# Optimization experiments

Hardware: AMD Instinct MI355X
Metric: run time of the kernel (lower is better)

The kernel has to match this reference:

```python
import math
import jax, jax.numpy as jnp
import numpy as np

D, H, NB, L, K = 45, 256, 6, 2, 8          # features, hidden, maf blocks, made hidden layers, spline bins
M = 3 * K - 1                               # params per feature (tails='linear')
TAIL = -math.log(1e-6)                      # tail_bound = -log(alpha)
MIN_BW = MIN_BH = MIN_D = 1e-3


def _masks():
    # nflows MADE sequential degrees (random_mask=False)
    d_in = np.arange(1, D + 1)
    d_h = (np.arange(H) % (D - 1)) + 1
    m0 = (d_h[:, None] >= d_in[None, :]).astype(np.float32)   # [H, D]
    mh = (d_h[:, None] >= d_h[None, :]).astype(np.float32)    # [H, H]
    d_out = np.repeat(d_in, M)                                 # nflows tile(): each degree repeated M times
    mf = (d_out[:, None] > d_h[None, :]).astype(np.float32)   # [D*M, H], strict for output layer
    return jnp.asarray(m0), jnp.asarray(mh), jnp.asarray(mf)


def _rq_spline(x, params):
    # x: [B, D]; params: [B, D, M]. unconstrained_rational_quadratic_spline, tails='linear'.
    uw = params[..., :K] / math.sqrt(H)        # nflows divides by sqrt(hidden_features)
    uh = params[..., K:2 * K] / math.sqrt(H)
    const = math.log(math.exp(1.0 - MIN_D) - 1.0)
    ud = jnp.pad(params[..., 2 * K:], ((0, 0), (0, 0), (1, 1)), constant_values=const)  # [B,D,K+1]
    inside = (x >= -TAIL) & (x <= TAIL)
    xc = jnp.clip(x, -TAIL, TAIL)

    def bin_edges(u, mn):
        p = jax.nn.softmax(u, -1)
        p = mn + (1.0 - mn * K) * p
        c = jnp.pad(jnp.cumsum(p, -1), ((0, 0), (0, 0), (1, 0)))
        c = 2.0 * TAIL * c - TAIL
        c = c.at[..., 0].set(-TAIL).at[..., -1].set(TAIL)
        return c, c[..., 1:] - c[..., :-1]

    cw, w = bin_edges(uw, MIN_BW)              # cumwidths [B,D,K+1], widths [B,D,K]
    ch, h = bin_edges(uh, MIN_BH)
    d = MIN_D + jax.nn.softplus(ud)            # derivatives [B,D,K+1]

    idx = jnp.clip(jnp.sum((xc[..., None] >= cw), -1) - 1, 0, K - 1)[..., None]
    g = lambda a: jnp.take_along_axis(a, idx, -1)[..., 0]
    icw, ibw, ich, ih = g(cw[..., :-1]), g(w), g(ch[..., :-1]), g(h)
    idelta = g(h / w)
    id0, id1 = g(d[..., :-1]), g(d[..., 1:])

    th = (xc - icw) / ibw
    th1 = th * (1.0 - th)
    den = idelta + (id0 + id1 - 2.0 * idelta) * th1
    y = ich + ih * (idelta * th * th + id0 * th1) / den
    lad = jnp.log(idelta * idelta * (id1 * th * th + 2.0 * idelta * th1 + id0 * (1.0 - th) ** 2)) - 2.0 * jnp.log(den)
    return jnp.where(inside, y, x), jnp.where(inside, lad, 0.0)


def setup_inputs() -> dict:
    key = jax.random.key(0)
    ks = jax.random.split(key, 10)
    B, s = 32768, 0.02
    return {
        "x": jax.random.normal(ks[0], (B, D), jnp.float32),
        "cond": jax.random.normal(ks[1], (B, 1), jnp.float32),
        "W0": jax.random.normal(ks[2], (NB, H, D), jnp.float32) * s,
        "b0": jax.random.normal(ks[3], (NB, H), jnp.float32) * s,
        "Wc": jax.random.normal(ks[4], (NB, H, 1), jnp.float32) * s,
        "bc": jax.random.normal(ks[5], (NB, H), jnp.float32) * s,
        "Wh": jax.random.normal(ks[6], (NB, L, H, H), jnp.float32) * s,
        "bh": jax.random.normal(ks[7], (NB, L, H), jnp.float32) * s,
        "Wf": jax.random.normal(ks[8], (NB, D * M, H), jnp.float32) * s,
        "bf": jax.random.normal(ks[9], (NB, D * M), jnp.float32) * s,
    }


def reference(x, cond, W0, b0, Wc, bc, Wh, bh, Wf, bf):
    m0, mh, mf = _masks()
    z = x
    ld = jnp.zeros(x.shape[0], x.dtype)
    for b in range(NB):  # CompositeTransform of NB MAF blocks
        hid = z @ (W0[b] * m0).T + b0[b] + cond @ Wc[b].T + bc[b]
        for l in range(L):  # MaskedFeedforwardBlock: linear -> ReLU (dropout=0, no BN)
            hid = jax.nn.relu(hid @ (Wh[b, l] * mh).T + bh[b, l])
        params = (hid @ (Wf[b] * mf).T + bf[b]).reshape(z.shape[0], D, M)
        z, lad = _rq_spline(z, params)
        ld = ld + lad.sum(-1)
    log_z = 0.5 * D * math.log(2.0 * math.pi)
    return -0.5 * jnp.sum(z * z, axis=1) - log_z + ld
```

## Files before the change

### kernel.cpp

```cpp
#include <hip/hip_runtime.h>


typedef __bf16 bf16;
typedef __bf16 bf16x8 __attribute__((ext_vector_type(8)));
typedef float  f32x16 __attribute__((ext_vector_type(16)));

#define TAILF  13.815510557964274f
#define LOGZ   41.352233994210265f

#define WS_W0M   0
#define WS_WHM   196608
#define WS_WFM   1769472
#define WS_BEFF  5210112
#define WS_BFP   5216256
#define WS_WCC   5243136
#define WS_NEED  5249280

#define N_W0  (6*256*64)
#define N_WH  (6*2*256*256)
#define N_WF  (6*5*224*256)
#define N_PREP (N_W0 + N_WH + N_WF)

__global__ void prep_all(const float* __restrict__ W0, const float* __restrict__ b0,
                         const float* __restrict__ Wc, const float* __restrict__ bc,
                         const float* __restrict__ Wh, const float* __restrict__ Wf,
                         const float* __restrict__ bfv,
                         bf16* __restrict__ W0m, bf16* __restrict__ Whm,
                         bf16* __restrict__ Wfm,
                         float* __restrict__ beff, float* __restrict__ bfp,
                         float* __restrict__ Wcc)
{
    int idx = blockIdx.x * 256 + threadIdx.x;
    if (idx < N_W0) {
        int j = idx & 7, lane = (idx >> 3) & 63, chunk = idx >> 9;
        int kt = chunk & 3, cg = (chunk >> 2) & 7, b = chunk >> 5;
        int col = cg * 32 + (lane & 31);
        int k   = kt * 16 + (lane >> 5) * 8 + j;
        float v = 0.f;
        if (k < 45 && (col % 44) >= k)
            v = W0[(b * 256 + col) * 45 + k];
        W0m[idx] = (bf16)v;
        if (k == 0) {
            beff[b * 256 + col] = b0[b * 256 + col] + bc[b * 256 + col];
            Wcc[b * 256 + col]  = Wc[b * 256 + col];
        }
    } else if (idx < N_W0 + N_WH) {
        int id = idx - N_W0;
        int j = id & 7, lane = (id >> 3) & 63, chunk = id >> 9;
        int kt = chunk & 15, cg = (chunk >> 4) & 7, bl = chunk >> 7;
        int col = cg * 32 + (lane & 31);
        int k   = kt * 16 + (lane >> 5) * 8 + j;
        float v = ((col % 44) >= (k % 44)) ? Wh[bl * 65536 + col * 256 + k] : 0.f;
        Whm[id] = (bf16)v;
    } else if (idx < N_PREP) {
        int id = idx - (N_W0 + N_WH);
        int j = id & 7, lane = (id >> 3) & 63, chunk = id >> 9;
        int kt = chunk & 15, t2 = chunk >> 4;
        int cg = t2 % 7, bg = t2 / 7;
        int b  = bg / 5, g = bg - 5 * b;
        int col = cg * 32 + (lane & 31);
        int k   = kt * 16 + (lane >> 5) * 8 + j;
        int f   = 9 * g + col / 23;
        int m   = col - (col / 23) * 23;
        bool valid = (col < 207);
        float v = 0.f;
        if (valid && (f > (k % 44)))
            v = Wf[(b * 1035 + f * 23 + m) * 256 + k];
        Wfm[id] = (bf16)v;
        if (k == 0)
            bfp[bg * 224 + col] = valid ? bfv[b * 1035 + f * 23 + m] : 0.f;
    }
}

#define SO_ZF    0
#define SO_ZB    11776
#define SO_HIDA  20992
#define SO_PBUF  54784
#define SO_COND  81408
#define SO_LD    81664
#define SMEM_BYTES 81920

template<int KT, int NACT, int MODE, int LIMIT>
__device__ __forceinline__ void gemm32(
    const bf16* Asrc, int lda,
    const bf16* __restrict__ Wp,
    const float* __restrict__ bias, const float* __restrict__ wcol,
    const float* condl, bf16* dst, int ldd,
    int w, int lane, bool preEpiSync)
{
    const bool act  = (w < NACT);
    const int  l31  = lane & 31;
    const int  kh8  = (lane >> 5) * 8;
    const bf16* Bp  = Wp + ((size_t)w * KT) * 512 + lane * 8;
    const bf16* Ap  = Asrc + l31 * lda + kh8;

    f32x16 acc0 = {}, acc1 = {};
    constexpr int CH = (KT < 8) ? KT : 8;
    #pragma unroll
    for (int khb = 0; khb < KT / CH; ++khb) {
        bf16x8 bq[CH];
        if (act) {
            #pragma unroll
            for (int c = 0; c < CH; ++c)
                bq[c] = *reinterpret_cast<const bf16x8*>(Bp + (khb * CH + c) * 512);
            #pragma unroll
            for (int c = 0; c < CH; ++c) {
                int kt = khb * CH + c;
                bf16x8 a0 = *reinterpret_cast<const bf16x8*>(Ap + kt * 16);
                bf16x8 a1 = *reinterpret_cast<const bf16x8*>(Ap + 32 * lda + kt * 16);
                acc0 = __builtin_amdgcn_mfma_f32_32x32x16_bf16(a0, bq[c], acc0, 0, 0, 0);
                acc1 = __builtin_amdgcn_mfma_f32_32x32x16_bf16(a1, bq[c], acc1, 0, 0, 0);
            }
        }
    }

    if (preEpiSync) __syncthreads();

    if (act) {
        const int col = w * 32 + l31;
        if (NACT == 8 || col < LIMIT) {
            const float bv  = bias[col];
            const float wcv = (MODE == 0) ? wcol[col] : 0.f;
            #pragma unroll
            for (int r = 0; r < 16; ++r) {
                int row = (r & 3) + 8 * (r >> 2) + (kh8 >> 1);
                float v0 = acc0[r] + bv;
                float v1 = acc1[r] + bv;
                if (MODE == 0) { v0 += condl[row] * wcv; v1 += condl[row + 32] * wcv; }
                if (MODE == 1) { v0 = fmaxf(v0, 0.f);   v1 = fmaxf(v1, 0.f); }
                dst[row * ldd + col]        = (bf16)v0;
                dst[(row + 32) * ldd + col] = (bf16)v1;
            }
        }
    }
    __syncthreads();
}

template<int NF>
__device__ __forceinline__ void do_spline(int fb, float* zf, bf16* zb,
                                          const bf16* pbuf, float* ldl, int t)
{
    for (int task = t; task < 64 * NF; task += 512) {
        int r  = task / NF;
        int fl = task - r * NF;
        const bf16* pp = pbuf + r * 208 + fl * 23;
        float P[23];
        #pragma unroll
        for (int m = 0; m < 23; ++m) P[m] = (float)pp[m];

        float xin = zf[r * 46 + fb + fl];
        float xc  = fminf(fmaxf(xin, -TAILF), TAILF);
        bool inside = (xin >= -TAILF) && (xin <= TAILF);

        float mw = P[0];
        #pragma unroll
        for (int i = 1; i < 8; ++i) mw = fmaxf(mw, P[i]);
        float ew[8], sw = 0.f;
        #pragma unroll
        for (int i = 0; i < 8; ++i) { ew[i] = __expf((P[i] - mw) * 0.0625f); sw += ew[i]; }
        float rws = 0.992f / sw;
        float cw[9]; cw[0] = -TAILF;
        #pragma unroll
        for (int i = 0; i < 8; ++i)
            cw[i + 1] = cw[i] + 2.f * TAILF * (1e-3f + ew[i] * rws);
        cw[8] = TAILF;
        float wb[8];
        #pragma unroll
        for (int i = 0; i < 8; ++i) wb[i] = cw[i + 1] - cw[i];

        float mh = P[8];
        #pragma unroll
        for (int i = 1; i < 8; ++i) mh = fmaxf(mh, P[8 + i]);
        float eh[8], sh = 0.f;
        #pragma unroll
        for (int i = 0; i < 8; ++i) { eh[i] = __expf((P[8 + i] - mh) * 0.0625f); sh += eh[i]; }
        float rhs = 0.992f / sh;
        float ch[9]; ch[0] = -TAILF;
        #pragma unroll
        for (int i = 0; i < 8; ++i)
            ch[i + 1] = ch[i] + 2.f * TAILF * (1e-3f + eh[i] * rhs);
        ch[8] = TAILF;
        float hb[8];
        #pragma unroll
        for (int i = 0; i < 8; ++i) hb[i] = ch[i + 1] - ch[i];

        float dd[9];
        dd[0] = 1.0f; dd[8] = 1.0f;
        #pragma unroll
        for (int i = 1; i < 8; ++i)
            dd[i] = 1e-3f + __logf(1.f + __expf(P[15 + i]));

        float icw = cw[0], ich = ch[0], ibw = wb[0], ibh = hb[0];
        float id0 = dd[0], id1 = dd[1];
        #pragma unroll
        for (int i = 1; i < 8; ++i) {
            bool ge = xc >= cw[i];
            icw = ge ? cw[i] : icw;  ich = ge ? ch[i] : ich;
            ibw = ge ? wb[i] : ibw;  ibh = ge ? hb[i] : ibh;
            id0 = ge ? dd[i] : id0;  id1 = ge ? dd[i + 1] : id1;
        }

        float th  = (xc - icw) / ibw;
        float th1 = th * (1.f - th);
        float dl  = ibh / ibw;
        float den = dl + (id0 + id1 - 2.f * dl) * th1;
        float yy  = ich + ibh * (dl * th * th + id0 * th1) / den;
        float num = dl * dl * (id1 * th * th + 2.f * dl * th1
                               + id0 * (1.f - th) * (1.f - th));
        float lad = __logf(num) - 2.f * __logf(den);

        if (inside) {
            zf[r * 46 + fb + fl] = yy;
            zb[r * 72 + fb + fl] = (bf16)yy;
            atomicAdd(&ldl[r], lad);
        }
    }
}

__global__ __launch_bounds__(512, 4) void maf_main(
    const float* __restrict__ x, const float* __restrict__ cond,
    const float* __restrict__ bh_all,
    const bf16* __restrict__ W0m, const bf16* __restrict__ Whm,
    const bf16* __restrict__ Wfm,
    const float* __restrict__ beff, const float* __restrict__ bfp,
    const float* __restrict__ Wcc,
    float* __restrict__ out, int B)
{
    extern __shared__ char smem[];
    float* zf    = (float*)(smem + SO_ZF);
    bf16*  zb    = (bf16*)(smem + SO_ZB);
    bf16*  hidA  = (bf16*)(smem + SO_HIDA);
    bf16*  pbuf  = (bf16*)(smem + SO_PBUF);
    float* condl = (float*)(smem + SO_COND);
    float* ldl   = (float*)(smem + SO_LD);

    const int t    = threadIdx.x;
    const int r0   = blockIdx.x * 64;
    const int w    = t >> 6;
    const int lane = t & 63;

    for (int i = t; i < 64 * 27; i += 512) {
        int r = i / 27, c = i - (i / 27) * 27;
        zb[r * 72 + 45 + c] = (bf16)0.f;
    }
    for (int i = t; i < 64 * 45; i += 512) {
        int r = i / 45, f = i - (i / 45) * 45;
        float v = (r0 + r < B) ? x[(size_t)(r0 + r) * 45 + f] : 0.f;
        zf[r * 46 + f] = v;
        zb[r * 72 + f] = (bf16)v;
    }
    if (t < 64) {
        condl[t] = (r0 + t < B) ? cond[r0 + t] : 0.f;
        ldl[t]   = 0.f;
    }
    __syncthreads();

    #pragma unroll 1
    for (int b = 0; b < 6; ++b) {
        gemm32<4, 8, 0, 256>(zb, 72, W0m + b * 16384,
                             beff + b * 256, Wcc + b * 256, condl,
                             hidA, 264, w, lane, false);
        #pragma unroll 1
        for (int l = 0; l < 2; ++l)
            gemm32<16, 8, 1, 256>(hidA, 264, Whm + (b * 2 + l) * 65536,
                                  bh_all + (b * 2 + l) * 256, nullptr, condl,
                                  hidA, 264, w, lane, true);
        #pragma unroll 1
        for (int g = 0; g < 5; ++g) {
            gemm32<16, 7, 2, 208>(hidA, 264, Wfm + (size_t)(b * 5 + g) * 57344,
                                  bfp + (b * 5 + g) * 224, nullptr, condl,
                                  pbuf, 208, w, lane, false);
            do_spline<9>(g * 9, zf, zb, pbuf, ldl, t);
            __syncthreads();
        }
    }

    if (t < 64 && r0 + t < B) {
        float s = 0.f;
        #pragma unroll
        for (int f = 0; f < 45; ++f) { float v = zf[t * 46 + f]; s += v * v; }
        out[r0 + t] = -0.5f * s - LOGZ + ldl[t];
    }
}

extern "C" void kernel_launch(void* const* d_in, const int* in_sizes, int n_in,
                              void* d_out, int out_size, void* d_ws, size_t ws_size,
                              hipStream_t stream)
{
    const float* x    = (const float*)d_in[0];
    const float* cond = (const float*)d_in[1];
    const float* W0   = (const float*)d_in[2];
    const float* b0   = (const float*)d_in[3];
    const float* Wc   = (const float*)d_in[4];
    const float* bc   = (const float*)d_in[5];
    const float* Wh   = (const float*)d_in[6];
    const float* bh   = (const float*)d_in[7];
    const float* Wf   = (const float*)d_in[8];
    const float* bfv  = (const float*)d_in[9];
    float* out = (float*)d_out;

    const int B = in_sizes[0] / 45;
    if (ws_size < (size_t)WS_NEED) return;

    char* ws = (char*)d_ws;
    bf16*  W0m  = (bf16*)(ws + WS_W0M);
    bf16*  Whm  = (bf16*)(ws + WS_WHM);
    bf16*  Wfm  = (bf16*)(ws + WS_WFM);
    float* beff = (float*)(ws + WS_BEFF);
    float* bfp  = (float*)(ws + WS_BFP);
    float* Wcc  = (float*)(ws + WS_WCC);

    prep_all<<<(N_PREP + 255) / 256, 256, 0, stream>>>(
        W0, b0, Wc, bc, Wh, Wf, bfv, W0m, Whm, Wfm, beff, bfp, Wcc);

    (void)hipFuncSetAttribute((const void*)maf_main,
                              hipFuncAttributeMaxDynamicSharedMemorySize,
                              SMEM_BYTES);

    const int nwg = (B + 63) / 64;
    maf_main<<<nwg, 512, SMEM_BYTES, stream>>>(
        x, cond, bh, W0m, Whm, Wfm, beff, bfp, Wcc, out, B);
}
```

Before: 375.0 us.

## Transpose MFMA operand roles, vectorize epilogue, pad spline params, drop softmax max

Weights become the MFMA A operand and activations the B operand. Each wave now owns 32 rows and two 32-column tiles, so the epilogue writes packed bf16x4 rows with vectorized bias loads. The first layer reads the fp32 z buffer directly, which removes the separate bf16 copy of z, and cuts its K tiles from 4 to 3. Spline params are padded to 24 per feature so they can be read with 16-byte loads. The spline also drops the softmax max-subtraction and swaps divisions for reciprocals; this risks overflow if the logits are large and adds some rounding error.

Result: slower. 435.5 us (+16.1%).

```diff
diff --git a/kernel.cpp b/kernel.cpp
--- a/kernel.cpp
+++ b/kernel.cpp
@@ -2,23 +2,25 @@
 
 
 typedef __bf16 bf16;
+typedef __bf16 bf16x4 __attribute__((ext_vector_type(4)));
 typedef __bf16 bf16x8 __attribute__((ext_vector_type(8)));
+typedef float  f32x4  __attribute__((ext_vector_type(4)));
 typedef float  f32x16 __attribute__((ext_vector_type(16)));
 
 #define TAILF  13.815510557964274f
 #define LOGZ   41.352233994210265f
 
 #define WS_W0M   0
-#define WS_WHM   196608
-#define WS_WFM   1769472
-#define WS_BEFF  5210112
-#define WS_BFP   5216256
-#define WS_WCC   5243136
-#define WS_NEED  5249280
-
-#define N_W0  (6*256*64)
+#define WS_WHM   147456
+#define WS_WFM   1720320
+#define WS_BEFF  5160960
+#define WS_BFP   5167104
+#define WS_WCC   5193984
+#define WS_NEED  5200128
+
+#define N_W0  (6*8*3*512)
 #define N_WH  (6*2*256*256)
-#define N_WF  (6*5*224*256)
+#define N_WF  (30*7*16*512)
 #define N_PREP (N_W0 + N_WH + N_WF)
 
 __global__ void prep_all(const float* __restrict__ W0, const float* __restrict__ b0,
@@ -33,8 +35,8 @@
     int idx = blockIdx.x * 256 + threadIdx.x;
     if (idx < N_W0) {
         int j = idx & 7, lane = (idx >> 3) & 63, chunk = idx >> 9;
-        int kt = chunk & 3, cg = (chunk >> 2) & 7, b = chunk >> 5;
-        int col = cg * 32 + (lane & 31);
+        int kt = chunk % 3, t = (chunk / 3) & 7, b = chunk / 24;
+        int col = t * 32 + (lane & 31);
         int k   = kt * 16 + (lane >> 5) * 8 + j;
         float v = 0.f;
         if (k < 45 && (col % 44) >= k)
@@ -47,8 +49,8 @@
     } else if (idx < N_W0 + N_WH) {
         int id = idx - N_W0;
         int j = id & 7, lane = (id >> 3) & 63, chunk = id >> 9;
-        int kt = chunk & 15, cg = (chunk >> 4) & 7, bl = chunk >> 7;
-        int col = cg * 32 + (lane & 31);
+        int kt = chunk & 15, t = (chunk >> 4) & 7, bl = chunk >> 7;
+        int col = t * 32 + (lane & 31);
         int k   = kt * 16 + (lane >> 5) * 8 + j;
         float v = ((col % 44) >= (k % 44)) ? Wh[bl * 65536 + col * 256 + k] : 0.f;
         Whm[id] = (bf16)v;
@@ -56,13 +58,13 @@
         int id = idx - (N_W0 + N_WH);
         int j = id & 7, lane = (id >> 3) & 63, chunk = id >> 9;
         int kt = chunk & 15, t2 = chunk >> 4;
-        int cg = t2 % 7, bg = t2 / 7;
+        int t  = t2 % 7, bg = t2 / 7;
         int b  = bg / 5, g = bg - 5 * b;
-        int col = cg * 32 + (lane & 31);
+        int col = t * 32 + (lane & 31);
         int k   = kt * 16 + (lane >> 5) * 8 + j;
-        int f   = 9 * g + col / 23;
-        int m   = col - (col / 23) * 23;
-        bool valid = (col < 207);
+        int f   = 9 * g + col / 24;
+        int m   = col - (col / 24) * 24;
+        bool valid = (col < 216) && (m < 23);
         float v = 0.f;
         if (valid && (f > (k % 44)))
             v = Wf[(b * 1035 + f * 23 + m) * 256 + k];
@@ -73,92 +75,131 @@
 }
 
 #define SO_ZF    0
-#define SO_ZB    11776
-#define SO_HIDA  20992
-#define SO_PBUF  54784
-#define SO_COND  81408
-#define SO_LD    81664
-#define SMEM_BYTES 81920
-
-template<int KT, int NACT, int MODE, int LIMIT>
+#define SO_HIDA  12288
+#define SO_PBUF  46080
+#define SO_COND  73728
+#define SO_LD    73984
+#define SMEM_BYTES 74240
+
+template<int KT, int NT, int MODE, bool F32B, int LIMIT>
 __device__ __forceinline__ void gemm32(
-    const bf16* Asrc, int lda,
+    const void* Bact, int ldb,
     const bf16* __restrict__ Wp,
     const float* __restrict__ bias, const float* __restrict__ wcol,
-    const float* condl, bf16* dst, int ldd,
+    float condv, bf16* dst, int ldd,
     int w, int lane, bool preEpiSync)
 {
-    const bool act  = (w < NACT);
-    const int  l31  = lane & 31;
-    const int  kh8  = (lane >> 5) * 8;
-    const bf16* Bp  = Wp + ((size_t)w * KT) * 512 + lane * 8;
-    const bf16* Ap  = Asrc + l31 * lda + kh8;
+    const int cg  = w & 3;
+    const int rg  = w >> 2;
+    const int l31 = lane & 31;
+    const int q   = lane >> 5;
+    const int t0  = cg * 2, t1 = cg * 2 + 1;
+    const bool has1 = (NT == 8) || (t1 < NT);
+    const int row = rg * 32 + l31;
+
+    const bf16*  Bp  = (const bf16*)Bact + row * ldb + q * 8;
+    const float* Bpf = (const float*)Bact + row * ldb + q * 8;
+    const bf16*  A0  = Wp + ((size_t)t0 * KT) * 512 + lane * 8;
+    const bf16*  A1  = Wp + ((size_t)t1 * KT) * 512 + lane * 8;
 
     f32x16 acc0 = {}, acc1 = {};
-    constexpr int CH = (KT < 8) ? KT : 8;
+    constexpr int CH = (KT < 4) ? KT : 4;
     #pragma unroll
-    for (int khb = 0; khb < KT / CH; ++khb) {
-        bf16x8 bq[CH];
-        if (act) {
-            #pragma unroll
-            for (int c = 0; c < CH; ++c)
-                bq[c] = *reinterpret_cast<const bf16x8*>(Bp + (khb * CH + c) * 512);
-            #pragma unroll
-            for (int c = 0; c < CH; ++c) {
-                int kt = khb * CH + c;
-                bf16x8 a0 = *reinterpret_cast<const bf16x8*>(Ap + kt * 16);
-                bf16x8 a1 = *reinterpret_cast<const bf16x8*>(Ap + 32 * lda + kt * 16);
-                acc0 = __builtin_amdgcn_mfma_f32_32x32x16_bf16(a0, bq[c], acc0, 0, 0, 0);
-                acc1 = __builtin_amdgcn_mfma_f32_32x32x16_bf16(a1, bq[c], acc1, 0, 0, 0);
+    for (int kb = 0; kb < KT / CH; ++kb) {
+        bf16x8 wq0[CH], wq1[CH];
+        #pragma unroll
+        for (int c = 0; c < CH; ++c) {
+            wq0[c] = *reinterpret_cast<const bf16x8*>(A0 + (kb * CH + c) * 512);
+            if (has1)
+                wq1[c] = *reinterpret_cast<const bf16x8*>(A1 + (kb * CH + c) * 512);
+        }
+        #pragma unroll
+        for (int c = 0; c < CH; ++c) {
+            const int kt = kb * CH + c;
+            bf16x8 bfrag;
+            if constexpr (F32B) {
+                f32x4 fa = *reinterpret_cast<const f32x4*>(Bpf + kt * 16);
+                f32x4 fb = *reinterpret_cast<const f32x4*>(Bpf + kt * 16 + 4);
+                bfrag = (bf16x8){(bf16)fa[0], (bf16)fa[1], (bf16)fa[2], (bf16)fa[3],
+                                 (bf16)fb[0], (bf16)fb[1], (bf16)fb[2], (bf16)fb[3]};
+            } else {
+                bfrag = *reinterpret_cast<const bf16x8*>(Bp + kt * 16);
             }
+            acc0 = __builtin_amdgcn_mfma_f32_32x32x16_bf16(wq0[c], bfrag, acc0, 0, 0, 0);
+            if (has1)
+                acc1 = __builtin_amdgcn_mfma_f32_32x32x16_bf16(wq1[c], bfrag, acc1, 0, 0, 0);
         }
     }
 
     if (preEpiSync) __syncthreads();
 
-    if (act) {
-        const int col = w * 32 + l31;
-        if (NACT == 8 || col < LIMIT) {
-            const float bv  = bias[col];
-            const float wcv = (MODE == 0) ? wcol[col] : 0.f;
-            #pragma unroll
-            for (int r = 0; r < 16; ++r) {
-                int row = (r & 3) + 8 * (r >> 2) + (kh8 >> 1);
-                float v0 = acc0[r] + bv;
-                float v1 = acc1[r] + bv;
-                if (MODE == 0) { v0 += condl[row] * wcv; v1 += condl[row + 32] * wcv; }
-                if (MODE == 1) { v0 = fmaxf(v0, 0.f);   v1 = fmaxf(v1, 0.f); }
-                dst[row * ldd + col]        = (bf16)v0;
-                dst[(row + 32) * ldd + col] = (bf16)v1;
+    bf16* drow = dst + row * ldd;
+    #pragma unroll
+    for (int rr = 0; rr < 4; ++rr) {
+        {
+            const int colb = t0 * 32 + rr * 8 + q * 4;
+            if (LIMIT == 256 || colb < LIMIT) {
+                f32x4 bv = *reinterpret_cast<const f32x4*>(bias + colb);
+                f32x4 wc = {};
+                if (MODE == 0) wc = *reinterpret_cast<const f32x4*>(wcol + colb);
+                bf16x4 pk;
+                #pragma unroll
+                for (int i = 0; i < 4; ++i) {
+                    float v = acc0[rr * 4 + i] + bv[i];
+                    if (MODE == 0) v += condv * wc[i];
+                    if (MODE == 1) v = fmaxf(v, 0.f);
+                    pk[i] = (bf16)v;
+                }
+                *reinterpret_cast<bf16x4*>(drow + colb) = pk;
             }
         }
+        if (has1) {
+            const int colb = t1 * 32 + rr * 8 + q * 4;
+            if (LIMIT == 256 || colb < LIMIT) {
+                f32x4 bv = *reinterpret_cast<const f32x4*>(bias + colb);
+                f32x4 wc = {};
+                if (MODE == 0) wc = *reinterpret_cast<const f32x4*>(wcol + colb);
+                bf16x4 pk;
+                #pragma unroll
+                for (int i = 0; i < 4; ++i) {
+                    float v = acc1[rr * 4 + i] + bv[i];
+                    if (MODE == 0) v += condv * wc[i];
+                    if (MODE == 1) v = fmaxf(v, 0.f);
+                    pk[i] = (bf16)v;
+                }
+                *reinterpret_cast<bf16x4*>(drow + colb) = pk;
+            }
+        }
     }
     __syncthreads();
 }
 
-template<int NF>
-__device__ __forceinline__ void do_spline(int fb, float* zf, bf16* zb,
+__device__ __forceinline__ void do_spline(int fb, float* zf,
                                           const bf16* pbuf, float* ldl, int t)
 {
-    for (int task = t; task < 64 * NF; task += 512) {
-        int r  = task / NF;
-        int fl = task - r * NF;
-        const bf16* pp = pbuf + r * 208 + fl * 23;
-        float P[23];
-        #pragma unroll
-        for (int m = 0; m < 23; ++m) P[m] = (float)pp[m];
-
-        float xin = zf[r * 46 + fb + fl];
+    for (int task = t; task < 64 * 9; task += 512) {
+        int r  = task / 9;
+        int fl = task - r * 9;
+        const bf16* pp = pbuf + r * 216 + fl * 24;
+        bf16x8 p0 = *reinterpret_cast<const bf16x8*>(pp);
+        bf16x8 p1 = *reinterpret_cast<const bf16x8*>(pp + 8);
+        bf16x8 p2 = *reinterpret_cast<const bf16x8*>(pp + 16);
+        float P[24];
+        #pragma unroll
+        for (int m = 0; m < 8; ++m) {
+            P[m]      = (float)p0[m];
+            P[8 + m]  = (float)p1[m];
+            P[16 + m] = (float)p2[m];
+        }
+
+        float xin = zf[r * 48 + fb + fl];
         float xc  = fminf(fmaxf(xin, -TAILF), TAILF);
         bool inside = (xin >= -TAILF) && (xin <= TAILF);
 
-        float mw = P[0];
-        #pragma unroll
-        for (int i = 1; i < 8; ++i) mw = fmaxf(mw, P[i]);
         float ew[8], sw = 0.f;
         #pragma unroll
-        for (int i = 0; i < 8; ++i) { ew[i] = __expf((P[i] - mw) * 0.0625f); sw += ew[i]; }
-        float rws = 0.992f / sw;
+        for (int i = 0; i < 8; ++i) { ew[i] = __expf(P[i] * 0.0625f); sw += ew[i]; }
+        float rws = 0.992f * __frcp_rn(sw);
         float cw[9]; cw[0] = -TAILF;
         #pragma unroll
         for (int i = 0; i < 8; ++i)
@@ -168,13 +209,10 @@
         #pragma unroll
         for (int i = 0; i < 8; ++i) wb[i] = cw[i + 1] - cw[i];
 
-        float mh = P[8];
-        #pragma unroll
-        for (int i = 1; i < 8; ++i) mh = fmaxf(mh, P[8 + i]);
         float eh[8], sh = 0.f;
         #pragma unroll
-        for (int i = 0; i < 8; ++i) { eh[i] = __expf((P[8 + i] - mh) * 0.0625f); sh += eh[i]; }
-        float rhs = 0.992f / sh;
+        for (int i = 0; i < 8; ++i) { eh[i] = __expf(P[8 + i] * 0.0625f); sh += eh[i]; }
+        float rhs = 0.992f * __frcp_rn(sh);
         float ch[9]; ch[0] = -TAILF;
         #pragma unroll
         for (int i = 0; i < 8; ++i)
@@ -200,18 +238,19 @@
             id0 = ge ? dd[i] : id0;  id1 = ge ? dd[i + 1] : id1;
         }
 
-        float th  = (xc - icw) / ibw;
-        float th1 = th * (1.f - th);
-        float dl  = ibh / ibw;
-        float den = dl + (id0 + id1 - 2.f * dl) * th1;
-        float yy  = ich + ibh * (dl * th * th + id0 * th1) / den;
-        float num = dl * dl * (id1 * th * th + 2.f * dl * th1
-                               + id0 * (1.f - th) * (1.f - th));
-        float lad = __logf(num) - 2.f * __logf(den);
+        float ribw = __frcp_rn(ibw);
+        float th   = (xc - icw) * ribw;
+        float th1  = th * (1.f - th);
+        float dl   = ibh * ribw;
+        float den  = dl + (id0 + id1 - 2.f * dl) * th1;
+        float rden = __frcp_rn(den);
+        float yy   = ich + ibh * (dl * th * th + id0 * th1) * rden;
+        float num  = dl * dl * (id1 * th * th + 2.f * dl * th1
+                                + id0 * (1.f - th) * (1.f - th));
+        float lad  = __logf(num * rden * rden);
 
         if (inside) {
-            zf[r * 46 + fb + fl] = yy;
-            zb[r * 72 + fb + fl] = (bf16)yy;
+            zf[r * 48 + fb + fl] = yy;
             atomicAdd(&ldl[r], lad);
         }
     }
@@ -228,7 +267,6 @@
 {
     extern __shared__ char smem[];
     float* zf    = (float*)(smem + SO_ZF);
-    bf16*  zb    = (bf16*)(smem + SO_ZB);
     bf16*  hidA  = (bf16*)(smem + SO_HIDA);
     bf16*  pbuf  = (bf16*)(smem + SO_PBUF);
     float* condl = (float*)(smem + SO_COND);
@@ -239,15 +277,13 @@
     const int w    = t >> 6;
     const int lane = t & 63;
 
-    for (int i = t; i < 64 * 27; i += 512) {
-        int r = i / 27, c = i - (i / 27) * 27;
-        zb[r * 72 + 45 + c] = (bf16)0.f;
+    for (int i = t; i < 64 * 3; i += 512) {
+        int r = i / 3, c = i - (i / 3) * 3;
+        zf[r * 48 + 45 + c] = 0.f;
     }
     for (int i = t; i < 64 * 45; i += 512) {
         int r = i / 45, f = i - (i / 45) * 45;
-        float v = (r0 + r < B) ? x[(size_t)(r0 + r) * 45 + f] : 0.f;
-        zf[r * 46 + f] = v;
-        zb[r * 72 + f] = (bf16)v;
+        zf[r * 48 + f] = (r0 + r < B) ? x[(size_t)(r0 + r) * 45 + f] : 0.f;
     }
     if (t < 64) {
         condl[t] = (r0 + t < B) ? cond[r0 + t] : 0.f;
@@ -255,22 +291,25 @@
     }
     __syncthreads();
 
+    const float condv = condl[(w >> 2) * 32 + (lane & 31)];
+
     #pragma unroll 1
     for (int b = 0; b < 6; ++b) {
-        gemm32<4, 8, 0, 256>(zb, 72, W0m + b * 16384,
-                             beff + b * 256, Wcc + b * 256, condl,
-                             hidA, 264, w, lane, false);
+        gemm32<3, 8, 0, true, 256>(zf, 48, W0m + b * 12288,
+                                   beff + b * 256, Wcc + b * 256, condv,
+                                   hidA, 264, w, lane, false);
         #pragma unroll 1
         for (int l = 0; l < 2; ++l)
-            gemm32<16, 8, 1, 256>(hidA, 264, Whm + (b * 2 + l) * 65536,
-                                  bh_all + (b * 2 + l) * 256, nullptr, condl,
-                                  hidA, 264, w, lane, true);
+            gemm32<16, 8, 1, false, 256>(hidA, 264, Whm + (b * 2 + l) * 65536,
+                                         bh_all + (b * 2 + l) * 256, nullptr, 0.f,
+                                         hidA, 264, w, lane, true);
         #pragma unroll 1
         for (int g = 0; g < 5; ++g) {
-            gemm32<16, 7, 2, 208>(hidA, 264, Wfm + (size_t)(b * 5 + g) * 57344,
-                                  bfp + (b * 5 + g) * 224, nullptr, condl,
-                                  pbuf, 208, w, lane, false);
-            do_spline<9>(g * 9, zf, zb, pbuf, ldl, t);
+            gemm32<16, 7, 2, false, 216>(hidA, 264,
+                                         Wfm + (size_t)(b * 5 + g) * 57344,
+                                         bfp + (b * 5 + g) * 224, nullptr, 0.f,
+                                         pbuf, 216, w, lane, false);
+            do_spline(g * 9, zf, pbuf, ldl, t);
             __syncthreads();
         }
     }
@@ -278,7 +317,7 @@
     if (t < 64 && r0 + t < B) {
         float s = 0.f;
         #pragma unroll
-        for (int f = 0; f < 45; ++f) { float v = zf[t * 46 + f]; s += v * v; }
+        for (int f = 0; f < 45; ++f) { float v = zf[t * 48 + f]; s += v * v; }
         out[r0 + t] = -0.5f * s - LOGZ + ldl[t];
     }
 }
```
